# Kernel optimization log

Measured on AMD Instinct MI355X. Metric: run time of the kernel, lower is better.

## Reference

```python
import jax, jax.numpy as jnp
from jax import lax
import numpy as np

NUM_GROUPS = 8
MAX_ITER = 10


def setup_inputs() -> dict:
    key = jax.random.key(0)
    N, deg, q = 50000, 32, NUM_GROUPS
    m = N * deg // 2  # undirected edges
    rng = np.random.default_rng(0)
    u = rng.integers(0, N, m)
    v = (u + 1 + rng.integers(0, N - 1, m)) % N  # no self loops
    src = jnp.asarray(np.concatenate([u, v]), dtype=jnp.int32)  # [E=2m] directed
    dst = jnp.asarray(np.concatenate([v, u]), dtype=jnp.int32)
    k1, k2 = jax.random.split(key)
    msg_init = jax.random.uniform(k1, (2 * m, q), dtype=jnp.float32)
    psi_init = jax.random.uniform(k2, (N, q), dtype=jnp.float32)
    # beta_ast = log(q / (sqrt(c) - 1) + 1), as in __init__ with mean_degree=c
    beta = jnp.log(q / (jnp.sqrt(jnp.float32(deg)) - 1.0) + 1.0)[None]
    return {"msg_init": msg_init, "psi_init": psi_init, "beta": beta,
            "src": src, "dst": dst, "N": N}


def reference(msg_init, psi_init, beta, src, dst, N):
    E = src.shape[0]
    m = E // 2
    q = msg_init.shape[1]
    # reverse-edge index: edge e=(i->j) has reverse rev[e]=(j->i)
    rev = jnp.concatenate([jnp.arange(m, E), jnp.arange(m)])
    mean_w = float(E) / float(N * N)  # W.mean() for unweighted symmetric adjacency
    b = beta[0]
    # normalized random init (init_messages)
    msg = msg_init / msg_init.sum(1, keepdims=True)   # [E, q] message along each directed edge
    psi = psi_init / psi_init.sum(1, keepdims=True)   # [N, q]
    h0 = -b * mean_w * psi.sum(0)                      # [q] external field (init_h)
    ew = jnp.exp(b) - 1.0                              # exp(beta*W_ij)-1 with W_ij=1

    def step(carry, _):
        msg, psi, h = carry
        logterm = jnp.log1p(msg * ew)                                  # [E, q]
        node_in = jax.ops.segment_sum(logterm, dst, num_segments=N)    # [N, q] sum over incoming edges
        # message i->j: product over neighbors k of i except j, times exp(h), normalized
        new_msg = jax.nn.softmax(node_in[src] - logterm[rev] + h, axis=-1)
        # marginal psi_i: product over all neighbors, times exp(h), normalized
        new_psi = jax.nn.softmax(node_in + h, axis=-1)
        new_h = -b * mean_w * new_psi.sum(0)
        return (new_msg, new_psi, new_h), None

    (msg, psi, h), _ = lax.scan(step, (msg, psi, h0), None, length=MAX_ITER)

    u, v = src[:m], dst[:m]  # undirected edge list
    # compute_reg: sum_e W_ij * ||psi_i - psi_j||^2 / m
    reg = jnp.sum((psi[u] - psi[v]) ** 2) / m
    # compute_modularity (argmax assignment, non-differentiable)
    assign = jnp.argmax(psi, axis=1)
    delta = (assign[u] == assign[v]).astype(jnp.float32)
    modularity = jnp.sum(delta * (1.0 - mean_w)) / m
    # entropy loss, scaled by 4*log(1/2)/log(1/q)
    H = -jnp.mean(jnp.sum(psi * jnp.log(psi + 1e-12), axis=1))
    entropy_loss = H * jnp.float32(4.0 * np.log(0.5) / np.log(1.0 / q))
    return psi, reg, entropy_loss, modularity
```

## Files before the change

### kernel.cpp

```cpp
#include <hip/hip_runtime.h>
#include <hip/hip_fp16.h>
#include <math.h>

#define Q 8
#define TPB 256
#define WPB (TPB / 64)
#define SCAN_T 1024

struct alignas(16) H8 { __half h[8]; };


__device__ __forceinline__ float fast_rcp(float x) {
  return __builtin_amdgcn_rcpf(x);
}

__device__ __forceinline__ void load8(const float* __restrict__ p, float r[Q]) {
  const float4* p4 = reinterpret_cast<const float4*>(p);
  float4 a = p4[0], b = p4[1];
  r[0]=a.x; r[1]=a.y; r[2]=a.z; r[3]=a.w;
  r[4]=b.x; r[5]=b.y; r[6]=b.z; r[7]=b.w;
}

__device__ __forceinline__ void store8h(__half* __restrict__ p, const float r[Q]) {
  H8 t;
#pragma unroll
  for (int j=0;j<Q;j++) t.h[j] = __float2half(r[j]);
  *reinterpret_cast<H8*>(p) = t;
}

__device__ __forceinline__ float wave_sum(float x) {
  x += __shfl_down(x, 32);
  x += __shfl_down(x, 16);
  x += __shfl_down(x, 8);
  x += __shfl_down(x, 4);
  x += __shfl_down(x, 2);
  x += __shfl_down(x, 1);
  return x;
}

__device__ __forceinline__ void block_reduce_atomic(float x, float* target, float* lds) {
  float w = wave_sum(x);
  const int lane = threadIdx.x & 63, wid = threadIdx.x >> 6;
  if (lane == 0) lds[wid] = w;
  __syncthreads();
  if (threadIdx.x == 0) {
    float t = 0.f;
#pragma unroll
    for (int i = 0; i < WPB; i++) t += lds[i];
    atomicAdd(target, t);
  }
  __syncthreads();
}

__device__ __forceinline__ float sum8_lanes(float x) {
  x += __shfl_xor(x, 1);
  x += __shfl_xor(x, 2);
  x += __shfl_xor(x, 4);
  return x;
}


__global__ void k_count_pos(const int* __restrict__ dst, int* __restrict__ cnt,
                            int* __restrict__ pos, int E) {
  int e = blockIdx.x * TPB + threadIdx.x;
  if (e < E) pos[e] = atomicAdd(&cnt[dst[e]], 1);
}

__global__ void k_scan1(const int* __restrict__ cnt, int* __restrict__ row_ptr,
                        int* __restrict__ bsum, int N) {
  __shared__ int lds[SCAN_T];
  const int tid = threadIdx.x;
  const int i = blockIdx.x * SCAN_T + tid;
  int c = (i < N) ? cnt[i] : 0;
  lds[tid] = c;
  __syncthreads();
  for (int off = 1; off < SCAN_T; off <<= 1) {
    int v = (tid >= off) ? lds[tid - off] : 0;
    __syncthreads();
    lds[tid] += v;
    __syncthreads();
  }
  if (i < N) row_ptr[i] = lds[tid] - c;
  if (tid == SCAN_T - 1) bsum[blockIdx.x] = lds[tid];
}

__global__ void k_scan2(const int* __restrict__ bsum, int* __restrict__ boffs,
                        int* __restrict__ row_ptr, int nb, int N) {
  __shared__ int lds[SCAN_T];
  const int tid = threadIdx.x;
  int v = (tid < nb) ? bsum[tid] : 0;
  lds[tid] = v;
  __syncthreads();
  for (int off = 1; off < SCAN_T; off <<= 1) {
    int t = (tid >= off) ? lds[tid - off] : 0;
    __syncthreads();
    lds[tid] += t;
    __syncthreads();
  }
  if (tid < nb) boffs[tid] = lds[tid] - v;
  if (tid == 0) row_ptr[N] = lds[nb - 1];
}

__global__ void k_scan3(int* __restrict__ row_ptr, const int* __restrict__ boffs, int N) {
  int i = blockIdx.x * SCAN_T + threadIdx.x;
  if (i < N) row_ptr[i] += boffs[blockIdx.x];
}

__global__ void k_rn_init(const int* __restrict__ src, const int* __restrict__ dst,
                          const int* __restrict__ pos,
                          const int* __restrict__ row_ptr,
                          const float* __restrict__ msg_init,
                          const float* __restrict__ beta,
                          int2* __restrict__ rn, __half* __restrict__ tA,
                          int E, int m) {
  int i = blockIdx.x * TPB + threadIdx.x;
  if (i >= m) return;
  const float b  = beta[0];
  const float ew = expf(b) - 1.0f;
  const int u = src[i], v = dst[i];
  const int pu = pos[i] + row_ptr[v];
  const int pv = pos[i + m] + row_ptr[u];
  int2 a; a.x = pv; a.y = u;
  int2 c; c.x = pu; c.y = v;
  rn[pu] = a;
  rn[pv] = c;

  float r0[Q], r1[Q];
  load8(msg_init + (size_t)i * Q, r0);
  load8(msg_init + ((size_t)i + (size_t)m) * Q, r1);
  float s0 = 0.f, s1 = 0.f;
#pragma unroll
  for (int j=0;j<Q;j++) { s0 += r0[j]; s1 += r1[j]; }
  float i0 = ew / s0, i1 = ew / s1;
#pragma unroll
  for (int j=0;j<Q;j++) { r0[j] = fmaf(r0[j], i0, 1.0f); r1[j] = fmaf(r1[j], i1, 1.0f); }
  store8h(tA + (size_t)pu * Q, r0);
  store8h(tA + (size_t)pv * Q, r1);
}


__global__ void k_pi0(const int* __restrict__ row_ptr, const __half* __restrict__ tA,
                      float* __restrict__ pi0, int N) {
  const int lane = threadIdx.x & 63;
  const int wid  = threadIdx.x >> 6;
  const int slot = lane >> 3;
  const int j    = lane & 7;
  const int wg = blockIdx.x * WPB + wid;
  const int ws = gridDim.x * WPB;
  for (int u = wg; u < N; u += ws) {
    const int s = row_ptr[u], e = row_ptr[u + 1];
    float prod = 1.f;
    for (int r = s + slot; r < e; r += 8) prod *= __half2float(tA[(size_t)r * Q + j]);
    prod *= __shfl_xor(prod, 8);
    prod *= __shfl_xor(prod, 16);
    prod *= __shfl_xor(prod, 32);
    if (slot == 0) pi0[(size_t)u * Q + j] = prod;
  }
}

__global__ void k_init_nodes(const float* __restrict__ psi_init,
                             float* __restrict__ S0, int N) {
  __shared__ float lds[WPB];
  int n = blockIdx.x * TPB + threadIdx.x;
  float p[Q];
  if (n < N) {
    load8(psi_init + (size_t)n * Q, p);
    float s = 0.f;
#pragma unroll
    for (int j=0;j<Q;j++) s += p[j];
    float inv = 1.0f / s;
#pragma unroll
    for (int j=0;j<Q;j++) p[j] *= inv;
  } else {
#pragma unroll
    for (int j=0;j<Q;j++) p[j] = 0.f;
  }
#pragma unroll
  for (int j=0;j<Q;j++) {
    block_reduce_atomic(p[j], &S0[j], lds);
  }
}

__global__ void k_iter(const int* __restrict__ row_ptr,
                       const int2* __restrict__ rn,
                       const __half* __restrict__ tIn,
                       __half* __restrict__ tOut,
                       const float* __restrict__ pi_cur,
                       float* __restrict__ pi_nxt,
                       const float* __restrict__ beta,
                       const float* __restrict__ S,
                       float* __restrict__ S_nxt,
                       float neg_mw, int N) {
  __shared__ float part[WPB][Q];
  const int lane = threadIdx.x & 63;
  const int wid  = threadIdx.x >> 6;
  const int slot = lane >> 3;
  const int j    = lane & 7;
  const float b  = beta[0];
  const float ew = expf(b) - 1.0f;
  const float eh = expf(neg_mw * b * S[j]);
  float sacc = 0.f;

  const int wg = blockIdx.x * WPB + wid;
  const int ws = gridDim.x * WPB;
  for (int u = wg; u < N; u += ws) {
    const int s = row_ptr[u], e = row_ptr[u + 1];
    float prod = 1.f;
    int r = s + slot;
    int2 w; float vin = 1.f, piv = 0.f;
    if (r < e) {
      w   = rn[r];
      vin = __half2float(tIn[(size_t)w.x * Q + j]);
      piv = pi_cur[(size_t)w.y * Q + j];
    }
    while (r < e) {
      const int r2 = r + 8;
      int2 w2; float vin2 = 1.f, piv2 = 0.f;
      if (r2 < e) {
        w2   = rn[r2];
        vin2 = __half2float(tIn[(size_t)w2.x * Q + j]);
        piv2 = pi_cur[(size_t)w2.y * Q + j];
      }
      const float num = piv * eh * fast_rcp(vin);
      const float sm  = sum8_lanes(num);
      const float pm  = num * fast_rcp(sm);
      const float tn  = fmaf(pm, ew, 1.0f);
      tOut[(size_t)r * Q + j] = __float2half(tn);
      prod *= tn;
      r = r2; w = w2; vin = vin2; piv = piv2;
    }
    prod *= __shfl_xor(prod, 8);
    prod *= __shfl_xor(prod, 16);
    prod *= __shfl_xor(prod, 32);
    if (slot == 0) {
      pi_nxt[(size_t)u * Q + j] = prod;
      const float pn = pi_cur[(size_t)u * Q + j] * eh;
      sacc += pn * fast_rcp(sum8_lanes(pn));
    }
  }
  if (slot == 0) part[wid][j] = sacc;
  __syncthreads();
  if (threadIdx.x < Q) {
    float tot = 0.f;
#pragma unroll
    for (int w = 0; w < WPB; w++) tot += part[w][threadIdx.x];
    atomicAdd(&S_nxt[threadIdx.x], tot);
  }
}


__global__ void k_psi_ent(const float* __restrict__ pi,
                          const float* __restrict__ beta,
                          const float* __restrict__ S,
                          float neg_mw, float* __restrict__ psi,
                          float* __restrict__ H_acc, int N) {
  __shared__ float lds[WPB];
  const int j = threadIdx.x & 7;
  const float eh = expf(neg_mw * beta[0] * S[j]);
  float hacc = 0.f;
  const int g0 = (blockIdx.x * TPB + threadIdx.x) >> 3;
  const int gs = (gridDim.x * TPB) >> 3;
  for (int n = g0; n < N; n += gs) {
    float pn = pi[(size_t)n * Q + j] * eh;
    float p = pn / sum8_lanes(pn);
    psi[(size_t)n * Q + j] = p;
    float el = p * logf(p + 1e-12f);
    el = sum8_lanes(el);
    if (j == 0) hacc += el;
  }
  block_reduce_atomic(hacc, H_acc, lds);
}

__global__ void k_edge_stats(const float* __restrict__ psi,
                             const int* __restrict__ src,
                             const int* __restrict__ dst,
                             float* __restrict__ reg_acc,
                             float* __restrict__ mod_acc,
                             float one_minus_mw, int m) {
  __shared__ float lds1[WPB];
  __shared__ float lds2[WPB];
  float reg = 0.f, mod = 0.f;
  for (int i = blockIdx.x * TPB + threadIdx.x; i < m; i += gridDim.x * TPB) {
    int u = src[i], v = dst[i];
    float pu[Q], pv[Q];
    load8(psi + (size_t)u * Q, pu);
    load8(psi + (size_t)v * Q, pv);
#pragma unroll
    for (int j=0;j<Q;j++) { float d = pu[j] - pv[j]; reg += d * d; }
    int au = 0, av = 0;
    float mu = pu[0], mv = pv[0];
#pragma unroll
    for (int j=1;j<Q;j++) {
      if (pu[j] > mu) { mu = pu[j]; au = j; }
      if (pv[j] > mv) { mv = pv[j]; av = j; }
    }
    if (au == av) mod += one_minus_mw;
  }
  block_reduce_atomic(reg, reg_acc, lds1);
  block_reduce_atomic(mod, mod_acc, lds2);
}

__global__ void k_finalize(const float* __restrict__ H_acc,
                           const float* __restrict__ reg_acc,
                           const float* __restrict__ mod_acc,
                           float* __restrict__ out3,
                           float inv_m, float inv_N, float entc) {
  out3[0] = reg_acc[0] * inv_m;
  out3[1] = (-H_acc[0] * inv_N) * entc;
  out3[2] = mod_acc[0] * inv_m;
}


extern "C" void kernel_launch(void* const* d_in, const int* in_sizes, int n_in,
                              void* d_out, int out_size, void* d_ws, size_t ws_size,
                              hipStream_t stream) {
  const float* msg_init = (const float*)d_in[0];
  const float* psi_init = (const float*)d_in[1];
  const float* beta     = (const float*)d_in[2];
  const int*   src      = (const int*)d_in[3];
  const int*   dst      = (const int*)d_in[4];

  const int E = in_sizes[3];
  const int m = E / 2;
  const int N = in_sizes[1] / Q;
  const double mean_w = (double)E / ((double)N * (double)N);
  const float  neg_mw = (float)(-mean_w);

  float* out = (float*)d_out;

  __half* tA = (__half*)d_ws;
  __half* tB = tA + (size_t)E * Q;
  int2*  rn   = (int2*)(tB + (size_t)E * Q);
  int*   pos  = (int*)(rn + E);
  int*   row_ptr = pos + E;
  int*   cnt     = row_ptr + (N + 1);
  int*   bsum    = cnt + N;
  int*   boffs   = bsum + SCAN_T;
  float* pi0     = (float*)(boffs + SCAN_T);
  float* pi1     = pi0 + (size_t)N * Q;
  float* S       = pi1 + (size_t)N * Q;
  float* H_acc   = S + 11 * Q;
  float* reg_acc = H_acc + 1;
  float* mod_acc = H_acc + 2;

  const int gridE = (E + TPB - 1) / TPB;
  const int gridM = (m + TPB - 1) / TPB;
  const int gridN = (N + TPB - 1) / TPB;
  const int gridI = min(2048, (N + WPB - 1) / WPB);
  const int gridS = min(512, gridM);
  const int nb    = (N + SCAN_T - 1) / SCAN_T;

  const float entc  = (float)(4.0 * log(0.5) / log(1.0 / (double)Q));
  const float inv_m = (float)(1.0 / (double)m);
  const float inv_N = (float)(1.0 / (double)N);
  const float omw   = (float)(1.0 - mean_w);

  hipMemsetAsync(cnt, 0, (size_t)N * sizeof(int), stream);
  hipMemsetAsync(S, 0, (size_t)(11 * Q + 3) * sizeof(float), stream);

  k_count_pos<<<gridE, TPB, 0, stream>>>(dst, cnt, pos, E);
  k_scan1<<<nb, SCAN_T, 0, stream>>>(cnt, row_ptr, bsum, N);
  k_scan2<<<1, SCAN_T, 0, stream>>>(bsum, boffs, row_ptr, nb, N);
  k_scan3<<<nb, SCAN_T, 0, stream>>>(row_ptr, boffs, N);
  k_rn_init<<<gridM, TPB, 0, stream>>>(src, dst, pos, row_ptr, msg_init, beta,
                                       rn, tA, E, m);
  k_pi0<<<gridI, TPB, 0, stream>>>(row_ptr, tA, pi0, N);
  k_init_nodes<<<gridN, TPB, 0, stream>>>(psi_init, S, N);

  __half* tcur = tA; __half* tnxt = tB;
  float*  pcur = pi0; float* pnxt = pi1;
  for (int t = 0; t < 9; ++t) {
    k_iter<<<gridI, TPB, 0, stream>>>(row_ptr, rn, tcur, tnxt, pcur, pnxt,
                                      beta, S + t * Q, S + (t + 1) * Q, neg_mw, N);
    __half* th = tcur; tcur = tnxt; tnxt = th;
    float*  pf = pcur; pcur = pnxt; pnxt = pf;
  }

  k_psi_ent<<<gridN, TPB, 0, stream>>>(pcur, beta, S + 9 * Q, neg_mw, out, H_acc, N);
  k_edge_stats<<<gridS, TPB, 0, stream>>>(out, src, dst, reg_acc, mod_acc, omw, m);
  k_finalize<<<1, 1, 0, stream>>>(H_acc, reg_acc, mod_acc, out + (size_t)N * Q,
                                  inv_m, inv_N, entc);
}
```

Measured before the change: 825.6 us.

## Store normalized cavity messages and process one node per 8-lane group with 16-byte rows

```diff
diff --git a/kernel.cpp b/kernel.cpp
--- a/kernel.cpp
+++ b/kernel.cpp
@@ -62,8 +62,17 @@
 
 __global__ void k_count_pos(const int* __restrict__ dst, int* __restrict__ cnt,
                             int* __restrict__ pos, int E) {
-  int e = blockIdx.x * TPB + threadIdx.x;
-  if (e < E) pos[e] = atomicAdd(&cnt[dst[e]], 1);
+  int i0 = (blockIdx.x * TPB + threadIdx.x) * 4;
+  if (i0 + 3 < E) {
+    int4 d = *reinterpret_cast<const int4*>(dst + i0);
+    int p0 = atomicAdd(&cnt[d.x], 1);
+    int p1 = atomicAdd(&cnt[d.y], 1);
+    int p2 = atomicAdd(&cnt[d.z], 1);
+    int p3 = atomicAdd(&cnt[d.w], 1);
+    *reinterpret_cast<int4*>(pos + i0) = make_int4(p0, p1, p2, p3);
+  } else {
+    for (int e = i0; e < E; e++) pos[e] = atomicAdd(&cnt[dst[e]], 1);
+  }
 }
 
 __global__ void k_scan1(const int* __restrict__ cnt, int* __restrict__ row_ptr,
@@ -106,13 +115,11 @@
   if (i < N) row_ptr[i] += boffs[blockIdx.x];
 }
 
-__global__ void k_rn_init(const int* __restrict__ src, const int* __restrict__ dst,
-                          const int* __restrict__ pos,
-                          const int* __restrict__ row_ptr,
-                          const float* __restrict__ msg_init,
-                          const float* __restrict__ beta,
-                          int2* __restrict__ rn, __half* __restrict__ tA,
-                          int E, int m) {
+__global__ void k_build(const int* __restrict__ src, const int* __restrict__ dst,
+                        const int* __restrict__ pos, const int* __restrict__ row_ptr,
+                        const float* __restrict__ msg_init,
+                        const float* __restrict__ beta,
+                        int* __restrict__ rev, __half* __restrict__ t0, int m) {
   int i = blockIdx.x * TPB + threadIdx.x;
   if (i >= m) return;
   const float b  = beta[0];
@@ -120,10 +127,8 @@
   const int u = src[i], v = dst[i];
   const int pu = pos[i] + row_ptr[v];
   const int pv = pos[i + m] + row_ptr[u];
-  int2 a; a.x = pv; a.y = u;
-  int2 c; c.x = pu; c.y = v;
-  rn[pu] = a;
-  rn[pv] = c;
+  rev[pu] = pv;
+  rev[pv] = pu;
 
   float r0[Q], r1[Q];
   load8(msg_init + (size_t)i * Q, r0);
@@ -134,27 +139,47 @@
   float i0 = ew / s0, i1 = ew / s1;
 #pragma unroll
   for (int j=0;j<Q;j++) { r0[j] = fmaf(r0[j], i0, 1.0f); r1[j] = fmaf(r1[j], i1, 1.0f); }
-  store8h(tA + (size_t)pu * Q, r0);
-  store8h(tA + (size_t)pv * Q, r1);
-}
-
-
-__global__ void k_pi0(const int* __restrict__ row_ptr, const __half* __restrict__ tA,
-                      float* __restrict__ pi0, int N) {
-  const int lane = threadIdx.x & 63;
-  const int wid  = threadIdx.x >> 6;
-  const int slot = lane >> 3;
-  const int j    = lane & 7;
-  const int wg = blockIdx.x * WPB + wid;
-  const int ws = gridDim.x * WPB;
-  for (int u = wg; u < N; u += ws) {
-    const int s = row_ptr[u], e = row_ptr[u + 1];
-    float prod = 1.f;
-    for (int r = s + slot; r < e; r += 8) prod *= __half2float(tA[(size_t)r * Q + j]);
-    prod *= __shfl_xor(prod, 8);
-    prod *= __shfl_xor(prod, 16);
-    prod *= __shfl_xor(prod, 32);
-    if (slot == 0) pi0[(size_t)u * Q + j] = prod;
+  store8h(t0 + (size_t)pu * Q, r0);
+  store8h(t0 + (size_t)pv * Q, r1);
+}
+
+
+__global__ void k_pi0cav(const int* __restrict__ row_ptr, const __half* __restrict__ t0,
+                         __half* __restrict__ cav0, float* __restrict__ pi0, int N) {
+  const int tid = threadIdx.x;
+  const int s = tid & 7;
+  const int u = (blockIdx.x * TPB + tid) >> 3;
+  if (u >= N) return;
+  const int st = row_ptr[u], en = row_ptr[u + 1];
+  float prod[Q];
+#pragma unroll
+  for (int j=0;j<Q;j++) prod[j] = 1.f;
+  for (int r = st + s; r < en; r += 8) {
+    H8 t = *reinterpret_cast<const H8*>(t0 + (size_t)r * Q);
+#pragma unroll
+    for (int j=0;j<Q;j++) prod[j] *= __half2float(t.h[j]);
+  }
+#pragma unroll
+  for (int j=0;j<Q;j++) {
+    prod[j] *= __shfl_xor(prod[j], 1);
+    prod[j] *= __shfl_xor(prod[j], 2);
+    prod[j] *= __shfl_xor(prod[j], 4);
+  }
+  if (s == 0) {
+    float4* o = reinterpret_cast<float4*>(pi0 + (size_t)u * Q);
+    o[0] = make_float4(prod[0], prod[1], prod[2], prod[3]);
+    o[1] = make_float4(prod[4], prod[5], prod[6], prod[7]);
+  }
+  for (int r = st + s; r < en; r += 8) {
+    H8 t = *reinterpret_cast<const H8*>(t0 + (size_t)r * Q);
+    float c[Q]; float sm = 0.f;
+#pragma unroll
+    for (int j=0;j<Q;j++) { c[j] = prod[j] * fast_rcp(__half2float(t.h[j])); sm += c[j]; }
+    float inv = fast_rcp(sm);
+    H8 o;
+#pragma unroll
+    for (int j=0;j<Q;j++) o.h[j] = __float2half(c[j] * inv);
+    *reinterpret_cast<H8*>(cav0 + (size_t)r * Q) = o;
   }
 }
 
@@ -181,70 +206,91 @@
   }
 }
 
-__global__ void k_iter(const int* __restrict__ row_ptr,
-                       const int2* __restrict__ rn,
-                       const __half* __restrict__ tIn,
-                       __half* __restrict__ tOut,
-                       const float* __restrict__ pi_cur,
-                       float* __restrict__ pi_nxt,
-                       const float* __restrict__ beta,
-                       const float* __restrict__ S,
-                       float* __restrict__ S_nxt,
-                       float neg_mw, int N) {
+__global__ void k_iter2(const int* __restrict__ row_ptr,
+                        const int* __restrict__ rev,
+                        const __half* __restrict__ cavIn,
+                        __half* __restrict__ cavOut,
+                        const float* __restrict__ pi_cur,
+                        float* __restrict__ pi_nxt,
+                        const float* __restrict__ beta,
+                        const float* __restrict__ S,
+                        float* __restrict__ S_nxt,
+                        float neg_mw, int N, int writeCav) {
   __shared__ float part[WPB][Q];
-  const int lane = threadIdx.x & 63;
-  const int wid  = threadIdx.x >> 6;
-  const int slot = lane >> 3;
-  const int j    = lane & 7;
+  const int tid = threadIdx.x;
+  const int s = tid & 7;
   const float b  = beta[0];
   const float ew = expf(b) - 1.0f;
-  const float eh = expf(neg_mw * b * S[j]);
+  const float hb = neg_mw * b;
+  float eh[Q];
+#pragma unroll
+  for (int j=0;j<Q;j++) eh[j] = expf(hb * S[j]);
+  const float ehs = expf(hb * S[s]);
   float sacc = 0.f;
 
-  const int wg = blockIdx.x * WPB + wid;
-  const int ws = gridDim.x * WPB;
-  for (int u = wg; u < N; u += ws) {
-    const int s = row_ptr[u], e = row_ptr[u + 1];
-    float prod = 1.f;
-    int r = s + slot;
-    int2 w; float vin = 1.f, piv = 0.f;
-    if (r < e) {
-      w   = rn[r];
-      vin = __half2float(tIn[(size_t)w.x * Q + j]);
-      piv = pi_cur[(size_t)w.y * Q + j];
-    }
-    while (r < e) {
-      const int r2 = r + 8;
-      int2 w2; float vin2 = 1.f, piv2 = 0.f;
-      if (r2 < e) {
-        w2   = rn[r2];
-        vin2 = __half2float(tIn[(size_t)w2.x * Q + j]);
-        piv2 = pi_cur[(size_t)w2.y * Q + j];
+  const int u = (blockIdx.x * TPB + tid) >> 3;
+  if (u < N) {
+    const int st = row_ptr[u], en = row_ptr[u + 1];
+    float prod[Q];
+#pragma unroll
+    for (int j=0;j<Q;j++) prod[j] = 1.f;
+    for (int r = st + s; r < en; r += 8) {
+      const int rv = rev[r];
+      H8 c = *reinterpret_cast<const H8*>(cavIn + (size_t)rv * Q);
+      float num[Q]; float sm = 0.f;
+#pragma unroll
+      for (int j=0;j<Q;j++) { num[j] = eh[j] * __half2float(c.h[j]); sm += num[j]; }
+      const float inv = fast_rcp(sm) * ew;
+      H8 o;
+#pragma unroll
+      for (int j=0;j<Q;j++) {
+        float tn = fmaf(num[j], inv, 1.0f);
+        prod[j] *= tn;
+        o.h[j] = __float2half(tn);
       }
-      const float num = piv * eh * fast_rcp(vin);
-      const float sm  = sum8_lanes(num);
-      const float pm  = num * fast_rcp(sm);
-      const float tn  = fmaf(pm, ew, 1.0f);
-      tOut[(size_t)r * Q + j] = __float2half(tn);
-      prod *= tn;
-      r = r2; w = w2; vin = vin2; piv = piv2;
-    }
-    prod *= __shfl_xor(prod, 8);
-    prod *= __shfl_xor(prod, 16);
-    prod *= __shfl_xor(prod, 32);
-    if (slot == 0) {
-      pi_nxt[(size_t)u * Q + j] = prod;
-      const float pn = pi_cur[(size_t)u * Q + j] * eh;
-      sacc += pn * fast_rcp(sum8_lanes(pn));
-    }
-  }
-  if (slot == 0) part[wid][j] = sacc;
+      *reinterpret_cast<H8*>(cavOut + (size_t)r * Q) = o;
+    }
+#pragma unroll
+    for (int j=0;j<Q;j++) {
+      prod[j] *= __shfl_xor(prod[j], 1);
+      prod[j] *= __shfl_xor(prod[j], 2);
+      prod[j] *= __shfl_xor(prod[j], 4);
+    }
+    if (s == 0) {
+      float4* o = reinterpret_cast<float4*>(pi_nxt + (size_t)u * Q);
+      o[0] = make_float4(prod[0], prod[1], prod[2], prod[3]);
+      o[1] = make_float4(prod[4], prod[5], prod[6], prod[7]);
+    }
+    {
+      float pn = pi_cur[(size_t)u * Q + s] * ehs;
+      float smp = sum8_lanes(pn);
+      sacc = pn * fast_rcp(smp);
+    }
+    if (writeCav) {
+      for (int r = st + s; r < en; r += 8) {
+        H8 t = *reinterpret_cast<const H8*>(cavOut + (size_t)r * Q);
+        float c[Q]; float sm = 0.f;
+#pragma unroll
+        for (int j=0;j<Q;j++) { c[j] = prod[j] * fast_rcp(__half2float(t.h[j])); sm += c[j]; }
+        const float inv = fast_rcp(sm);
+        H8 o;
+#pragma unroll
+        for (int j=0;j<Q;j++) o.h[j] = __float2half(c[j] * inv);
+        *reinterpret_cast<H8*>(cavOut + (size_t)r * Q) = o;
+      }
+    }
+  }
+  sacc += __shfl_xor(sacc, 8);
+  sacc += __shfl_xor(sacc, 16);
+  sacc += __shfl_xor(sacc, 32);
+  const int lane = tid & 63, wid = tid >> 6;
+  if (lane < Q) part[wid][lane] = sacc;
   __syncthreads();
-  if (threadIdx.x < Q) {
+  if (tid < Q) {
     float tot = 0.f;
 #pragma unroll
-    for (int w = 0; w < WPB; w++) tot += part[w][threadIdx.x];
-    atomicAdd(&S_nxt[threadIdx.x], tot);
+    for (int w = 0; w < WPB; w++) tot += part[w][tid];
+    atomicAdd(&S_nxt[tid], tot);
   }
 }
 
@@ -328,10 +374,10 @@
 
   float* out = (float*)d_out;
 
-  __half* tA = (__half*)d_ws;
-  __half* tB = tA + (size_t)E * Q;
-  int2*  rn   = (int2*)(tB + (size_t)E * Q);
-  int*   pos  = (int*)(rn + E);
+  __half* cavA = (__half*)d_ws;
+  __half* cavB = cavA + (size_t)E * Q;
+  int*   rev     = (int*)(cavB + (size_t)E * Q);
+  int*   pos     = rev + E;
   int*   row_ptr = pos + E;
   int*   cnt     = row_ptr + (N + 1);
   int*   bsum    = cnt + N;
@@ -343,10 +389,10 @@
   float* reg_acc = H_acc + 1;
   float* mod_acc = H_acc + 2;
 
-  const int gridE = (E + TPB - 1) / TPB;
+  const int gridC = (E + TPB * 4 - 1) / (TPB * 4);
   const int gridM = (m + TPB - 1) / TPB;
   const int gridN = (N + TPB - 1) / TPB;
-  const int gridI = min(2048, (N + WPB - 1) / WPB);
+  const int gridG = (N * Q + TPB - 1) / TPB;
   const int gridS = min(512, gridM);
   const int nb    = (N + SCAN_T - 1) / SCAN_T;
 
@@ -358,21 +404,22 @@
   hipMemsetAsync(cnt, 0, (size_t)N * sizeof(int), stream);
   hipMemsetAsync(S, 0, (size_t)(11 * Q + 3) * sizeof(float), stream);
 
-  k_count_pos<<<gridE, TPB, 0, stream>>>(dst, cnt, pos, E);
+  k_count_pos<<<gridC, TPB, 0, stream>>>(dst, cnt, pos, E);
   k_scan1<<<nb, SCAN_T, 0, stream>>>(cnt, row_ptr, bsum, N);
   k_scan2<<<1, SCAN_T, 0, stream>>>(bsum, boffs, row_ptr, nb, N);
   k_scan3<<<nb, SCAN_T, 0, stream>>>(row_ptr, boffs, N);
-  k_rn_init<<<gridM, TPB, 0, stream>>>(src, dst, pos, row_ptr, msg_init, beta,
-                                       rn, tA, E, m);
-  k_pi0<<<gridI, TPB, 0, stream>>>(row_ptr, tA, pi0, N);
+  k_build<<<gridM, TPB, 0, stream>>>(src, dst, pos, row_ptr, msg_init, beta,
+                                     rev, cavB, m);
+  k_pi0cav<<<gridG, TPB, 0, stream>>>(row_ptr, cavB, cavA, pi0, N);
   k_init_nodes<<<gridN, TPB, 0, stream>>>(psi_init, S, N);
 
-  __half* tcur = tA; __half* tnxt = tB;
-  float*  pcur = pi0; float* pnxt = pi1;
+  __half* ccur = cavA; __half* cnxt = cavB;
+  float*  pcur = pi0;  float*  pnxt = pi1;
   for (int t = 0; t < 9; ++t) {
-    k_iter<<<gridI, TPB, 0, stream>>>(row_ptr, rn, tcur, tnxt, pcur, pnxt,
-                                      beta, S + t * Q, S + (t + 1) * Q, neg_mw, N);
-    __half* th = tcur; tcur = tnxt; tnxt = th;
+    k_iter2<<<gridG, TPB, 0, stream>>>(row_ptr, rev, ccur, cnxt, pcur, pnxt,
+                                       beta, S + t * Q, S + (t + 1) * Q,
+                                       neg_mw, N, (t < 8) ? 1 : 0);
+    __half* ch = ccur; ccur = cnxt; cnxt = ch;
     float*  pf = pcur; pcur = pnxt; pnxt = pf;
   }
 
```

Result: faster. 740.6 us (-10.3%).
